# Performance work log

Hardware: AMD Instinct MI355X
Metric: run time of the kernel (lower is better)

The kernel has to match this reference:

```python
import jax, jax.numpy as jnp
import numpy as np
from jax import lax

N = 4096          # n_nodes
D_IN = 64         # node_attr_size
H = 64            # hidden_size
MAX_ITER = 10


def setup_inputs() -> dict:
    key = jax.random.key(0)
    ks = jax.random.split(key, 6)
    # Scale L and recurrent weights so the tanh fixed-point iteration is well-behaved
    X = jax.random.normal(ks[0], (N, D_IN), dtype=jnp.float32)
    L = jax.random.normal(ks[1], (N, N), dtype=jnp.float32) / jnp.sqrt(jnp.float32(N))
    W_ih0 = jax.random.normal(ks[2], (H, D_IN), dtype=jnp.float32) * 0.5
    W_hh0 = jax.random.normal(ks[3], (H, H), dtype=jnp.float32) * 0.5
    W_ih1 = jax.random.normal(ks[4], (H, H), dtype=jnp.float32) * 0.5
    W_hh1 = jax.random.normal(ks[5], (H, H), dtype=jnp.float32) * 0.5
    return {"X": X, "L": L, "W_ih0": W_ih0, "W_hh0": W_hh0,
            "W_ih1": W_ih1, "W_hh1": W_hh1}


def _gesn_layer(x, L, W_ih, W_hh):
    # wiu = linear(X, W_ih) computed once; then iterate
    # h <- tanh(wiu + L @ (h @ W_hh^T)) for max_iter steps (fixed-count
    # version of the torch convergence loop; see notes).
    wiu = x @ W_ih.T                                   # [N, H]
    h0 = jnp.zeros((x.shape[0], W_hh.shape[0]), x.dtype)

    def step(h, _):
        z = wiu + L @ (h @ W_hh.T)                     # [N, H]
        return jnp.tanh(z), None

    h, _ = lax.scan(step, h0, None, length=MAX_ITER)
    return h


def reference(X, L, W_ih0, W_hh0, W_ih1, W_hh1):
    h1 = _gesn_layer(X, L, W_ih0, W_hh0)               # layer 0: [N, H]
    h2 = _gesn_layer(h1, L, W_ih1, W_hh1)              # layer 1: [N, H]
    return jnp.concatenate([h1, h2], axis=-1)          # [N, 2H]
```

## Files before the change

### kernel.cpp

```cpp
#include <hip/hip_runtime.h>
#include <hip/hip_bf16.h>
#include <math.h>


#define NN 4096
#define HH 64

typedef float  f32x4  __attribute__((ext_vector_type(4)));
typedef short  bf16x8 __attribute__((ext_vector_type(8)));

static __device__ __forceinline__ unsigned short bf16_bits(__hip_bfloat16 b) {
    union { __hip_bfloat16 b; unsigned short u; } cv; cv.b = b; return cv.u;
}

__global__ __launch_bounds__(256) void convert_L(
    const float* __restrict__ L, short* __restrict__ Ahi, short* __restrict__ Alo)
{
    __shared__ float T[16 * 132];
    const int t  = threadIdx.x;
    const int rb = blockIdx.x >> 5;
    const int kg = blockIdx.x & 31;

    {
        const int row = t >> 4;
        const int c4  = (t & 15) * 4;
        const float* src = L + (size_t)(rb * 16 + row) * NN + kg * 128;
        float4 v0 = *reinterpret_cast<const float4*>(src + c4);
        float4 v1 = *reinterpret_cast<const float4*>(src + c4 + 64);
        *reinterpret_cast<float4*>(&T[row * 132 + c4])      = v0;
        *reinterpret_cast<float4*>(&T[row * 132 + c4 + 64]) = v1;
    }
    __syncthreads();

    const int kbl = t >> 6;
    const int l   = t & 63;
    const int r   = l & 15, g = l >> 4;
    short hi8[8], lo8[8];
#pragma unroll
    for (int j = 0; j < 8; ++j) {
        const float v = T[r * 132 + kbl * 32 + g * 8 + j];
        __hip_bfloat16 bh = __float2bfloat16(v);
        const float vh = __bfloat162float(bh);
        __hip_bfloat16 bl = __float2bfloat16(v - vh);
        hi8[j] = (short)bf16_bits(bh);
        lo8[j] = (short)bf16_bits(bl);
    }
    const size_t off = ((size_t)(rb * 128 + kg * 4 + kbl) * 64 + l) * 8;
    *reinterpret_cast<bf16x8*>(Ahi + off) = *reinterpret_cast<bf16x8*>(hi8);
    *reinterpret_cast<bf16x8*>(Alo + off) = *reinterpret_cast<bf16x8*>(lo8);
}

__global__ __launch_bounds__(512) void gesn_mm(
    const short* __restrict__ Ahi, const short* __restrict__ Alo,
    const short* __restrict__ Bhi, const short* __restrict__ Blo,
    float* __restrict__ Gp)
{
    __shared__ short Bh_lds[16 * 4 * 64 * 8];
    __shared__ short Bl_lds[16 * 4 * 64 * 8];

    const int t = threadIdx.x;
    const int w = t >> 6, l = t & 63;
    const int p = blockIdx.x >> 3;
    const int s = blockIdx.x & 7;
    const int rb = p * 8 + w;
    const int kb0 = s * 16;

    {
        const short* srcH = Bhi + (size_t)kb0 * 4 * 64 * 8;
        const short* srcL = Blo + (size_t)kb0 * 4 * 64 * 8;
#pragma unroll
        for (int q = 0; q < 8; ++q) {
            const int idx = (q * 512 + t) * 8;
            *reinterpret_cast<bf16x8*>(&Bh_lds[idx]) =
                *reinterpret_cast<const bf16x8*>(srcH + idx);
            *reinterpret_cast<bf16x8*>(&Bl_lds[idx]) =
                *reinterpret_cast<const bf16x8*>(srcL + idx);
        }
    }
    __syncthreads();

    const size_t abase = ((size_t)(rb * 128 + kb0) * 64 + l) * 8;
    bf16x8 aH[16], aL[16];
#pragma unroll
    for (int q = 0; q < 16; ++q) {
        aH[q] = *reinterpret_cast<const bf16x8*>(Ahi + abase + (size_t)q * 512);
        aL[q] = *reinterpret_cast<const bf16x8*>(Alo + abase + (size_t)q * 512);
    }

    f32x4 accP[4] = {};
    f32x4 accQ[4] = {};

#pragma unroll
    for (int kbl = 0; kbl < 16; ++kbl) {
        bf16x8 bH[4], bL[4];
#pragma unroll
        for (int cf = 0; cf < 4; ++cf) {
            const int idx = ((kbl * 4 + cf) * 64 + l) * 8;
            bH[cf] = *reinterpret_cast<const bf16x8*>(&Bh_lds[idx]);
            bL[cf] = *reinterpret_cast<const bf16x8*>(&Bl_lds[idx]);
        }
#pragma unroll
        for (int cf = 0; cf < 4; ++cf) {
            accP[cf] = __builtin_amdgcn_mfma_f32_16x16x32_bf16(
                aH[kbl], bH[cf], accP[cf], 0, 0, 0);
            accQ[cf] = __builtin_amdgcn_mfma_f32_16x16x32_bf16(
                aH[kbl], bL[cf], accQ[cf], 0, 0, 0);
            accQ[cf] = __builtin_amdgcn_mfma_f32_16x16x32_bf16(
                aL[kbl], bH[cf], accQ[cf], 0, 0, 0);
        }
    }

    float* g = Gp + (size_t)s * NN * HH;
    const int col0  = l & 15;
    const int rbase = (l >> 4) * 4;
#pragma unroll
    for (int cf = 0; cf < 4; ++cf)
#pragma unroll
        for (int r = 0; r < 4; ++r)
            g[(size_t)(rb * 16 + rbase + r) * HH + cf * 16 + col0]
                = accP[cf][r] + accQ[cf][r];
}

__global__ __launch_bounds__(256) void gesn_post(
    const float* __restrict__ Gsrc, int nsplit,
    const float* __restrict__ wiu_in, float* __restrict__ wiu_out,
    const float* __restrict__ W,
    float* __restrict__ hf32,
    short* __restrict__ Bhi, short* __restrict__ Blo,
    float* __restrict__ out2, int outc0)
{
    __shared__ float W_lds[64 * 65];
    __shared__ float G_lds[16 * 68];
    __shared__ unsigned short Hi_lds[16][66];
    __shared__ unsigned short Lo_lds[16][66];
    const int t = threadIdx.x;

    {
        const int j  = t >> 2;
        const int k0 = (t & 3) << 4;
#pragma unroll
        for (int q = 0; q < 16; ++q)
            W_lds[j * 65 + k0 + q] = W[j * 64 + k0 + q];
    }
    const int r0 = blockIdx.x * 16;

    {
        const int row = t >> 4;
        const int c4  = (t & 15) * 4;
        float4 sum;
        if (nsplit == 0) {
            sum = *reinterpret_cast<const float4*>(
                Gsrc + (size_t)(r0 + row) * HH + c4);
        } else {
            sum = make_float4(0.f, 0.f, 0.f, 0.f);
            for (int sidx = 0; sidx < nsplit; ++sidx) {
                const float4 v = *reinterpret_cast<const float4*>(
                    Gsrc + (size_t)sidx * NN * HH + (size_t)(r0 + row) * HH + c4);
                sum.x += v.x; sum.y += v.y; sum.z += v.z; sum.w += v.w;
            }
        }
        *reinterpret_cast<float4*>(&G_lds[row * 68 + c4]) = sum;
    }
    __syncthreads();

    const int j  = t & 63;
    const int ig = t >> 6;
#pragma unroll
    for (int rr = 0; rr < 4; ++rr) {
        const int i = ig * 4 + rr;
        float z = wiu_in ? wiu_in[(size_t)(r0 + i) * HH + j] : 0.f;
#pragma unroll
        for (int m = 0; m < 64; ++m)
            z = fmaf(G_lds[i * 68 + m], W_lds[j * 65 + m], z);
        if (wiu_out) wiu_out[(size_t)(r0 + i) * HH + j] = z;
        const float hv = tanhf(z);
        hf32[(size_t)(r0 + i) * HH + j] = hv;
        if (out2) out2[(size_t)(r0 + i) * 128 + outc0 + j] = hv;
        __hip_bfloat16 bh = __float2bfloat16(hv);
        const float vh = __bfloat162float(bh);
        __hip_bfloat16 bl = __float2bfloat16(hv - vh);
        Hi_lds[i][j] = bf16_bits(bh);
        Lo_lds[i][j] = bf16_bits(bl);
    }
    __syncthreads();

    if (t < 128) {
        const int j2     = t & 63;
        const int glocal = t >> 6;
        const int kb     = r0 >> 5;
        const int gg     = ((r0 & 31) >> 3) + glocal;
        const int cf     = j2 >> 4;
        const int lane   = gg * 16 + (j2 & 15);
        short hi8[8], lo8[8];
#pragma unroll
        for (int jj = 0; jj < 8; ++jj) {
            const int i = glocal * 8 + jj;
            hi8[jj] = (short)Hi_lds[i][j2];
            lo8[jj] = (short)Lo_lds[i][j2];
        }
        const size_t off = ((size_t)(kb * 4 + cf) * 64 + lane) * 8;
        *reinterpret_cast<bf16x8*>(Bhi + off) = *reinterpret_cast<bf16x8*>(hi8);
        *reinterpret_cast<bf16x8*>(Blo + off) = *reinterpret_cast<bf16x8*>(lo8);
    }
}

__global__ __launch_bounds__(256) void gesn_input_kernel(
    const float* __restrict__ x, const float* __restrict__ W,
    float* __restrict__ wiu, float* __restrict__ h)
{
    __shared__ float W_lds[64 * 65];
    __shared__ float x_lds[256];
    const int t = threadIdx.x;
    {
        const int j  = t >> 2;
        const int k0 = (t & 3) << 4;
#pragma unroll
        for (int q = 0; q < 16; ++q)
            W_lds[j * 65 + k0 + q] = W[j * 64 + k0 + q];
    }
    const int i0 = blockIdx.x * 4;
    x_lds[t] = x[i0 * 64 + t];
    __syncthreads();
    const int j = t & 63, i = t >> 6;
    float z = 0.f;
#pragma unroll
    for (int k = 0; k < 64; ++k)
        z = fmaf(x_lds[i * 64 + k], W_lds[j * 65 + k], z);
    const int gidx = (i0 + i) * 64 + j;
    wiu[gidx] = z;
    h[gidx]   = tanhf(z);
}

__global__ __launch_bounds__(256) void gesn_iter_kernel(
    const float* __restrict__ L, const float* __restrict__ h_in,
    const float* __restrict__ wiu, const float* __restrict__ W,
    float* __restrict__ h_out, float* __restrict__ out2, int out_col0)
{
    __shared__ float h_lds[64 * 64];
    __shared__ float L_lds[16 * 68];
    __shared__ float G_lds[16 * 68];
    __shared__ float W_lds[64 * 65];
    const int t = threadIdx.x;
    {
        const int j  = t >> 2;
        const int k0 = (t & 3) << 4;
#pragma unroll
        for (int q = 0; q < 16; ++q)
            W_lds[j * 65 + k0 + q] = W[j * 64 + k0 + q];
    }
    const int r0 = blockIdx.x * 16;
    const int p  = t >> 5;
    const int c0 = (t & 31) * 2;
    float acc00 = 0.f, acc01 = 0.f, acc10 = 0.f, acc11 = 0.f;
    const int lr = t >> 4;
    const int lc = (t & 15) * 4;
    for (int kb = 0; kb < 64; ++kb) {
        __syncthreads();
        const float4 lv = *reinterpret_cast<const float4*>(
            &L[(size_t)(r0 + lr) * 4096 + kb * 64 + lc]);
        *reinterpret_cast<float4*>(&L_lds[lr * 68 + lc]) = lv;
        const float4* hsrc = reinterpret_cast<const float4*>(h_in + kb * 4096);
        float4* hdst = reinterpret_cast<float4*>(h_lds);
#pragma unroll
        for (int q = 0; q < 4; ++q)
            hdst[t + 256 * q] = hsrc[t + 256 * q];
        __syncthreads();
#pragma unroll
        for (int kk = 0; kk < 64; ++kk) {
            const float  lv0 = L_lds[(2 * p) * 68 + kk];
            const float  lv1 = L_lds[(2 * p + 1) * 68 + kk];
            const float2 hv  = *reinterpret_cast<const float2*>(&h_lds[kk * 64 + c0]);
            acc00 = fmaf(lv0, hv.x, acc00);
            acc01 = fmaf(lv0, hv.y, acc01);
            acc10 = fmaf(lv1, hv.x, acc10);
            acc11 = fmaf(lv1, hv.y, acc11);
        }
    }
    G_lds[(2 * p) * 68 + c0]         = acc00;
    G_lds[(2 * p) * 68 + c0 + 1]     = acc01;
    G_lds[(2 * p + 1) * 68 + c0]     = acc10;
    G_lds[(2 * p + 1) * 68 + c0 + 1] = acc11;
    __syncthreads();
    const int j  = t & 63;
    const int iw = t >> 6;
#pragma unroll
    for (int rr = 0; rr < 4; ++rr) {
        const int i = iw * 4 + rr;
        float z = wiu[(size_t)(r0 + i) * 64 + j];
#pragma unroll
        for (int m = 0; m < 64; ++m)
            z = fmaf(G_lds[i * 68 + m], W_lds[j * 65 + m], z);
        const float hv = tanhf(z);
        h_out[(size_t)(r0 + i) * 64 + j] = hv;
        if (out2) out2[(size_t)(r0 + i) * 128 + out_col0 + j] = hv;
    }
}

extern "C" void kernel_launch(void* const* d_in, const int* in_sizes, int n_in,
                              void* d_out, int out_size, void* d_ws, size_t ws_size,
                              hipStream_t stream) {
    const float* X    = (const float*)d_in[0];
    const float* L    = (const float*)d_in[1];
    const float* Wih0 = (const float*)d_in[2];
    const float* Whh0 = (const float*)d_in[3];
    const float* Wih1 = (const float*)d_in[4];
    const float* Whh1 = (const float*)d_in[5];
    float* out = (float*)d_out;
    char* ws = (char*)d_ws;

    const size_t MB = 1024 * 1024;
    const size_t need = 76 * MB;

    if (ws_size >= need) {
        short* Ahi = (short*)(ws);
        short* Alo = (short*)(ws + 32 * MB);
        short* Bhi = (short*)(ws + 64 * MB);
        short* Blo = (short*)(ws + 64 * MB + 512 * 1024);
        float* wiu = (float*)(ws + 65 * MB);
        float* hA  = (float*)(ws + 66 * MB);
        float* hB  = (float*)(ws + 67 * MB);
        float* Gp  = (float*)(ws + 68 * MB);

        convert_L<<<8192, 256, 0, stream>>>(L, Ahi, Alo);

        for (int layer = 0; layer < 2; ++layer) {
            const float* x   = layer ? hA : X;
            const float* Wih = layer ? Wih1 : Wih0;
            const float* Whh = layer ? Whh1 : Whh0;
            float* hcur = layer ? hB : hA;

            gesn_post<<<256, 256, 0, stream>>>(x, 0, nullptr, wiu, Wih,
                                               hcur, Bhi, Blo, nullptr, 0);
            for (int it = 0; it < 9; ++it) {
                gesn_mm<<<256, 512, 0, stream>>>(Ahi, Alo, Bhi, Blo, Gp);
                float* o2 = (it == 8) ? out : nullptr;
                gesn_post<<<256, 256, 0, stream>>>(Gp, 8, wiu, nullptr, Whh,
                                                   hcur, Bhi, Blo, o2, layer * 64);
            }
        }
    } else {
        float* wiu = (float*)(ws);
        float* hA  = (float*)(ws + (1u << 20));
        float* hB  = (float*)(ws + (2u << 20));
        for (int layer = 0; layer < 2; ++layer) {
            const float* x   = layer ? hB : X;
            const float* Wih = layer ? Wih1 : Wih0;
            const float* Whh = layer ? Whh1 : Whh0;
            gesn_input_kernel<<<1024, 256, 0, stream>>>(x, Wih, wiu, hA);
            float* cur = hA;
            float* nxt = hB;
            for (int it = 0; it < 9; ++it) {
                float* o2 = (it == 8) ? out : nullptr;
                gesn_iter_kernel<<<256, 256, 0, stream>>>(L, cur, wiu, Whh, nxt,
                                                          o2, layer * 64);
                float* tmp = cur; cur = nxt; nxt = tmp;
            }
        }
    }
}
```

Baseline: 509.4 us.

## Fuse iteration loop into persistent kernel with grid barriers and register-resident L

Replaces the roughly 38 separate matmul and post-processing launches with one persistent 256-block kernel that steps through both layers and all iterations, separated by software grid barriers built on atomics. Each block loads its slice of the split-bf16 L once into registers and keeps it across all 18 matmul phases, so L is no longer re-read from memory every iteration. The post phase now runs with 512 threads, each handling 2 rows instead of 4. This relies on all 256 blocks being co-resident, since otherwise the spin barrier deadlocks. It also pays for barrier latency and holds large register and LDS allocations.

```diff
diff --git a/kernel.cpp b/kernel.cpp
--- a/kernel.cpp
+++ b/kernel.cpp
@@ -5,6 +5,8 @@
 
 #define NN 4096
 #define HH 64
+#define NBLK 256
+#define TPB 512
 
 typedef float  f32x4  __attribute__((ext_vector_type(4)));
 typedef short  bf16x8 __attribute__((ext_vector_type(8)));
@@ -50,101 +52,52 @@
     *reinterpret_cast<bf16x8*>(Alo + off) = *reinterpret_cast<bf16x8*>(lo8);
 }
 
-__global__ __launch_bounds__(512) void gesn_mm(
-    const short* __restrict__ Ahi, const short* __restrict__ Alo,
-    const short* __restrict__ Bhi, const short* __restrict__ Blo,
-    float* __restrict__ Gp)
-{
-    __shared__ short Bh_lds[16 * 4 * 64 * 8];
-    __shared__ short Bl_lds[16 * 4 * 64 * 8];
-
-    const int t = threadIdx.x;
-    const int w = t >> 6, l = t & 63;
-    const int p = blockIdx.x >> 3;
-    const int s = blockIdx.x & 7;
-    const int rb = p * 8 + w;
-    const int kb0 = s * 16;
-
-    {
-        const short* srcH = Bhi + (size_t)kb0 * 4 * 64 * 8;
-        const short* srcL = Blo + (size_t)kb0 * 4 * 64 * 8;
-#pragma unroll
-        for (int q = 0; q < 8; ++q) {
-            const int idx = (q * 512 + t) * 8;
-            *reinterpret_cast<bf16x8*>(&Bh_lds[idx]) =
-                *reinterpret_cast<const bf16x8*>(srcH + idx);
-            *reinterpret_cast<bf16x8*>(&Bl_lds[idx]) =
-                *reinterpret_cast<const bf16x8*>(srcL + idx);
-        }
-    }
-    __syncthreads();
-
-    const size_t abase = ((size_t)(rb * 128 + kb0) * 64 + l) * 8;
-    bf16x8 aH[16], aL[16];
-#pragma unroll
-    for (int q = 0; q < 16; ++q) {
-        aH[q] = *reinterpret_cast<const bf16x8*>(Ahi + abase + (size_t)q * 512);
-        aL[q] = *reinterpret_cast<const bf16x8*>(Alo + abase + (size_t)q * 512);
-    }
-
-    f32x4 accP[4] = {};
-    f32x4 accQ[4] = {};
-
-#pragma unroll
-    for (int kbl = 0; kbl < 16; ++kbl) {
-        bf16x8 bH[4], bL[4];
-#pragma unroll
-        for (int cf = 0; cf < 4; ++cf) {
-            const int idx = ((kbl * 4 + cf) * 64 + l) * 8;
-            bH[cf] = *reinterpret_cast<const bf16x8*>(&Bh_lds[idx]);
-            bL[cf] = *reinterpret_cast<const bf16x8*>(&Bl_lds[idx]);
-        }
-#pragma unroll
-        for (int cf = 0; cf < 4; ++cf) {
-            accP[cf] = __builtin_amdgcn_mfma_f32_16x16x32_bf16(
-                aH[kbl], bH[cf], accP[cf], 0, 0, 0);
-            accQ[cf] = __builtin_amdgcn_mfma_f32_16x16x32_bf16(
-                aH[kbl], bL[cf], accQ[cf], 0, 0, 0);
-            accQ[cf] = __builtin_amdgcn_mfma_f32_16x16x32_bf16(
-                aL[kbl], bH[cf], accQ[cf], 0, 0, 0);
-        }
-    }
-
-    float* g = Gp + (size_t)s * NN * HH;
-    const int col0  = l & 15;
-    const int rbase = (l >> 4) * 4;
-#pragma unroll
-    for (int cf = 0; cf < 4; ++cf)
-#pragma unroll
-        for (int r = 0; r < 4; ++r)
-            g[(size_t)(rb * 16 + rbase + r) * HH + cf * 16 + col0]
-                = accP[cf][r] + accQ[cf][r];
-}
-
-__global__ __launch_bounds__(256) void gesn_post(
+__device__ __forceinline__ void grid_barrier(unsigned* cnt, unsigned* gen, int nb)
+{
+    __syncthreads();
+    if (threadIdx.x == 0) {
+        __threadfence();
+        unsigned g = __hip_atomic_load(gen, __ATOMIC_RELAXED,
+                                       __HIP_MEMORY_SCOPE_AGENT);
+        unsigned old = __hip_atomic_fetch_add(cnt, 1u, __ATOMIC_ACQ_REL,
+                                              __HIP_MEMORY_SCOPE_AGENT);
+        if (old == (unsigned)(nb - 1)) {
+            __hip_atomic_store(cnt, 0u, __ATOMIC_RELAXED,
+                               __HIP_MEMORY_SCOPE_AGENT);
+            __hip_atomic_fetch_add(gen, 1u, __ATOMIC_RELEASE,
+                                   __HIP_MEMORY_SCOPE_AGENT);
+        } else {
+            while (__hip_atomic_load(gen, __ATOMIC_ACQUIRE,
+                                     __HIP_MEMORY_SCOPE_AGENT) == g) {
+                __builtin_amdgcn_s_sleep(2);
+            }
+        }
+        __threadfence();
+    }
+    __syncthreads();
+}
+
+__device__ __forceinline__ void post_phase(
     const float* __restrict__ Gsrc, int nsplit,
     const float* __restrict__ wiu_in, float* __restrict__ wiu_out,
-    const float* __restrict__ W,
-    float* __restrict__ hf32,
+    const float* __restrict__ W, float* __restrict__ hf32,
     short* __restrict__ Bhi, short* __restrict__ Blo,
-    float* __restrict__ out2, int outc0)
-{
-    __shared__ float W_lds[64 * 65];
-    __shared__ float G_lds[16 * 68];
-    __shared__ unsigned short Hi_lds[16][66];
-    __shared__ unsigned short Lo_lds[16][66];
+    float* __restrict__ out2, int outc0, int r0, char* smem)
+{
+    float* W_lds = (float*)smem;
+    float* G_lds = (float*)(smem + 16640);
+    unsigned short* Hi_lds = (unsigned short*)(smem + 16640 + 4352);
+    unsigned short* Lo_lds = (unsigned short*)(smem + 16640 + 4352 + 2112);
     const int t = threadIdx.x;
 
     {
-        const int j  = t >> 2;
-        const int k0 = (t & 3) << 4;
-#pragma unroll
-        for (int q = 0; q < 16; ++q)
+        const int j  = t >> 3;
+        const int k0 = (t & 7) * 8;
+#pragma unroll
+        for (int q = 0; q < 8; ++q)
             W_lds[j * 65 + k0 + q] = W[j * 64 + k0 + q];
     }
-    const int r0 = blockIdx.x * 16;
-
-    {
+    if (t < 256) {
         const int row = t >> 4;
         const int c4  = (t & 15) * 4;
         float4 sum;
@@ -166,8 +119,8 @@
     const int j  = t & 63;
     const int ig = t >> 6;
 #pragma unroll
-    for (int rr = 0; rr < 4; ++rr) {
-        const int i = ig * 4 + rr;
+    for (int rr = 0; rr < 2; ++rr) {
+        const int i = ig * 2 + rr;
         float z = wiu_in ? wiu_in[(size_t)(r0 + i) * HH + j] : 0.f;
 #pragma unroll
         for (int m = 0; m < 64; ++m)
@@ -179,8 +132,8 @@
         __hip_bfloat16 bh = __float2bfloat16(hv);
         const float vh = __bfloat162float(bh);
         __hip_bfloat16 bl = __float2bfloat16(hv - vh);
-        Hi_lds[i][j] = bf16_bits(bh);
-        Lo_lds[i][j] = bf16_bits(bl);
+        Hi_lds[i * 66 + j] = bf16_bits(bh);
+        Lo_lds[i * 66 + j] = bf16_bits(bl);
     }
     __syncthreads();
 
@@ -195,12 +148,107 @@
 #pragma unroll
         for (int jj = 0; jj < 8; ++jj) {
             const int i = glocal * 8 + jj;
-            hi8[jj] = (short)Hi_lds[i][j2];
-            lo8[jj] = (short)Lo_lds[i][j2];
+            hi8[jj] = (short)Hi_lds[i * 66 + j2];
+            lo8[jj] = (short)Lo_lds[i * 66 + j2];
         }
         const size_t off = ((size_t)(kb * 4 + cf) * 64 + lane) * 8;
         *reinterpret_cast<bf16x8*>(Bhi + off) = *reinterpret_cast<bf16x8*>(hi8);
         *reinterpret_cast<bf16x8*>(Blo + off) = *reinterpret_cast<bf16x8*>(lo8);
+    }
+}
+
+__global__ __launch_bounds__(TPB, 2) void gesn_persistent(
+    const short* __restrict__ Ahi, const short* __restrict__ Alo,
+    short* __restrict__ Bhi, short* __restrict__ Blo,
+    const float* __restrict__ X,
+    const float* __restrict__ Wih0, const float* __restrict__ Whh0,
+    const float* __restrict__ Wih1, const float* __restrict__ Whh1,
+    float* __restrict__ wiu, float* __restrict__ hA, float* __restrict__ hB,
+    float* __restrict__ Gp, float* __restrict__ out,
+    unsigned* bar_cnt, unsigned* bar_gen)
+{
+    __shared__ char smem[131072];
+    const int t = threadIdx.x;
+    const int b = blockIdx.x;
+    const int w = t >> 6, l = t & 63;
+    const int p = b >> 3, s = b & 7;
+    const int rb  = p * 8 + w;
+    const int kb0 = s * 16;
+    const int r0  = b * 16;
+
+    const size_t abase = ((size_t)(rb * 128 + kb0) * 64 + l) * 8;
+    bf16x8 aH[16], aL[16];
+#pragma unroll
+    for (int q = 0; q < 16; ++q) {
+        aH[q] = *reinterpret_cast<const bf16x8*>(Ahi + abase + (size_t)q * 512);
+        aL[q] = *reinterpret_cast<const bf16x8*>(Alo + abase + (size_t)q * 512);
+    }
+
+    for (int layer = 0; layer < 2; ++layer) {
+        const float* x   = layer ? hA : X;
+        const float* Wih = layer ? Wih1 : Wih0;
+        const float* Whh = layer ? Whh1 : Whh0;
+        float* hcur      = layer ? hB : hA;
+
+        post_phase(x, 0, nullptr, wiu, Wih, hcur, Bhi, Blo, nullptr, 0, r0, smem);
+        grid_barrier(bar_cnt, bar_gen, NBLK);
+
+        for (int it = 0; it < 9; ++it) {
+            short* Bh_lds = (short*)smem;
+            short* Bl_lds = (short*)(smem + 65536);
+            {
+                const short* srcH = Bhi + (size_t)kb0 * 4 * 64 * 8;
+                const short* srcL = Blo + (size_t)kb0 * 4 * 64 * 8;
+#pragma unroll
+                for (int q = 0; q < 8; ++q) {
+                    const int idx = (q * 512 + t) * 8;
+                    *reinterpret_cast<bf16x8*>(&Bh_lds[idx]) =
+                        *reinterpret_cast<const bf16x8*>(srcH + idx);
+                    *reinterpret_cast<bf16x8*>(&Bl_lds[idx]) =
+                        *reinterpret_cast<const bf16x8*>(srcL + idx);
+                }
+            }
+            __syncthreads();
+
+            f32x4 accP[4] = {};
+            f32x4 accQ[4] = {};
+#pragma unroll
+            for (int kbl = 0; kbl < 16; ++kbl) {
+                bf16x8 bH[4], bL[4];
+#pragma unroll
+                for (int cf = 0; cf < 4; ++cf) {
+                    const int idx = ((kbl * 4 + cf) * 64 + l) * 8;
+                    bH[cf] = *reinterpret_cast<const bf16x8*>(&Bh_lds[idx]);
+                    bL[cf] = *reinterpret_cast<const bf16x8*>(&Bl_lds[idx]);
+                }
+#pragma unroll
+                for (int cf = 0; cf < 4; ++cf) {
+                    accP[cf] = __builtin_amdgcn_mfma_f32_16x16x32_bf16(
+                        aH[kbl], bH[cf], accP[cf], 0, 0, 0);
+                    accQ[cf] = __builtin_amdgcn_mfma_f32_16x16x32_bf16(
+                        aH[kbl], bL[cf], accQ[cf], 0, 0, 0);
+                    accQ[cf] = __builtin_amdgcn_mfma_f32_16x16x32_bf16(
+                        aL[kbl], bH[cf], accQ[cf], 0, 0, 0);
+                }
+            }
+            {
+                float* g = Gp + (size_t)s * NN * HH;
+                const int col0  = l & 15;
+                const int rbase = (l >> 4) * 4;
+#pragma unroll
+                for (int cf = 0; cf < 4; ++cf)
+#pragma unroll
+                    for (int r = 0; r < 4; ++r)
+                        g[(size_t)(rb * 16 + rbase + r) * HH + cf * 16 + col0]
+                            = accP[cf][r] + accQ[cf][r];
+            }
+            grid_barrier(bar_cnt, bar_gen, NBLK);
+
+            float* o2 = (it == 8) ? out : nullptr;
+            post_phase(Gp, 8, wiu, nullptr, Whh, hcur, Bhi, Blo,
+                       o2, layer * 64, r0, smem);
+            grid_barrier(bar_cnt, bar_gen, NBLK);
+        }
     }
 }
 
@@ -309,7 +357,7 @@
     char* ws = (char*)d_ws;
 
     const size_t MB = 1024 * 1024;
-    const size_t need = 76 * MB;
+    const size_t need = 77 * MB;
 
     if (ws_size >= need) {
         short* Ahi = (short*)(ws);
@@ -320,24 +368,14 @@
         float* hA  = (float*)(ws + 66 * MB);
         float* hB  = (float*)(ws + 67 * MB);
         float* Gp  = (float*)(ws + 68 * MB);
-
+        unsigned char* bar = (unsigned char*)(ws + 76 * MB);
+
+        hipMemsetAsync(bar, 0, 1024, stream);
         convert_L<<<8192, 256, 0, stream>>>(L, Ahi, Alo);
-
-        for (int layer = 0; layer < 2; ++layer) {
-            const float* x   = layer ? hA : X;
-            const float* Wih = layer ? Wih1 : Wih0;
-            const float* Whh = layer ? Whh1 : Whh0;
-            float* hcur = layer ? hB : hA;
-
-            gesn_post<<<256, 256, 0, stream>>>(x, 0, nullptr, wiu, Wih,
-                                               hcur, Bhi, Blo, nullptr, 0);
-            for (int it = 0; it < 9; ++it) {
-                gesn_mm<<<256, 512, 0, stream>>>(Ahi, Alo, Bhi, Blo, Gp);
-                float* o2 = (it == 8) ? out : nullptr;
-                gesn_post<<<256, 256, 0, stream>>>(Gp, 8, wiu, nullptr, Whh,
-                                                   hcur, Bhi, Blo, o2, layer * 64);
-            }
-        }
+        gesn_persistent<<<NBLK, TPB, 0, stream>>>(
+            Ahi, Alo, Bhi, Blo, X, Wih0, Whh0, Wih1, Whh1,
+            wiu, hA, hB, Gp, out,
+            (unsigned*)bar, (unsigned*)(bar + 256));
     } else {
         float* wiu = (float*)(ws);
         float* hA  = (float*)(ws + (1u << 20));
```

After: 1.465 ms. 2.88x slower.

## Fuse split-K matmul and tanh update into one kernel per iteration

Applied to the files above, without the earlier changes.

Merges the split-K MFMA matmul and the post-processing kernel into one kernel per iteration. Each block owns 16 rows, its 8 waves split K, and partial sums are reduced in shared memory rather than through an 8-way global partial buffer. The packed bf16 h is double-buffered because other blocks still read the input h while this block writes its output. This removes a launch and the global round trip for partials, but each block now reads all of B straight from global/L2 with no LDS staging, and there are only 256 blocks.

```diff
diff --git a/kernel.cpp b/kernel.cpp
--- a/kernel.cpp
+++ b/kernel.cpp
@@ -50,137 +50,106 @@
     *reinterpret_cast<bf16x8*>(Alo + off) = *reinterpret_cast<bf16x8*>(lo8);
 }
 
-__global__ __launch_bounds__(512) void gesn_mm(
-    const short* __restrict__ Ahi, const short* __restrict__ Alo,
-    const short* __restrict__ Bhi, const short* __restrict__ Blo,
-    float* __restrict__ Gp)
-{
-    __shared__ short Bh_lds[16 * 4 * 64 * 8];
-    __shared__ short Bl_lds[16 * 4 * 64 * 8];
-
-    const int t = threadIdx.x;
-    const int w = t >> 6, l = t & 63;
-    const int p = blockIdx.x >> 3;
-    const int s = blockIdx.x & 7;
-    const int rb = p * 8 + w;
-    const int kb0 = s * 16;
-
-    {
-        const short* srcH = Bhi + (size_t)kb0 * 4 * 64 * 8;
-        const short* srcL = Blo + (size_t)kb0 * 4 * 64 * 8;
-#pragma unroll
-        for (int q = 0; q < 8; ++q) {
-            const int idx = (q * 512 + t) * 8;
-            *reinterpret_cast<bf16x8*>(&Bh_lds[idx]) =
-                *reinterpret_cast<const bf16x8*>(srcH + idx);
-            *reinterpret_cast<bf16x8*>(&Bl_lds[idx]) =
-                *reinterpret_cast<const bf16x8*>(srcL + idx);
-        }
-    }
-    __syncthreads();
-
-    const size_t abase = ((size_t)(rb * 128 + kb0) * 64 + l) * 8;
-    bf16x8 aH[16], aL[16];
-#pragma unroll
-    for (int q = 0; q < 16; ++q) {
-        aH[q] = *reinterpret_cast<const bf16x8*>(Ahi + abase + (size_t)q * 512);
-        aL[q] = *reinterpret_cast<const bf16x8*>(Alo + abase + (size_t)q * 512);
-    }
-
-    f32x4 accP[4] = {};
-    f32x4 accQ[4] = {};
-
-#pragma unroll
-    for (int kbl = 0; kbl < 16; ++kbl) {
-        bf16x8 bH[4], bL[4];
-#pragma unroll
-        for (int cf = 0; cf < 4; ++cf) {
-            const int idx = ((kbl * 4 + cf) * 64 + l) * 8;
-            bH[cf] = *reinterpret_cast<const bf16x8*>(&Bh_lds[idx]);
-            bL[cf] = *reinterpret_cast<const bf16x8*>(&Bl_lds[idx]);
-        }
-#pragma unroll
-        for (int cf = 0; cf < 4; ++cf) {
-            accP[cf] = __builtin_amdgcn_mfma_f32_16x16x32_bf16(
-                aH[kbl], bH[cf], accP[cf], 0, 0, 0);
-            accQ[cf] = __builtin_amdgcn_mfma_f32_16x16x32_bf16(
-                aH[kbl], bL[cf], accQ[cf], 0, 0, 0);
-            accQ[cf] = __builtin_amdgcn_mfma_f32_16x16x32_bf16(
-                aL[kbl], bH[cf], accQ[cf], 0, 0, 0);
-        }
-    }
-
-    float* g = Gp + (size_t)s * NN * HH;
-    const int col0  = l & 15;
-    const int rbase = (l >> 4) * 4;
-#pragma unroll
-    for (int cf = 0; cf < 4; ++cf)
-#pragma unroll
-        for (int r = 0; r < 4; ++r)
-            g[(size_t)(rb * 16 + rbase + r) * HH + cf * 16 + col0]
-                = accP[cf][r] + accQ[cf][r];
-}
-
-__global__ __launch_bounds__(256) void gesn_post(
-    const float* __restrict__ Gsrc, int nsplit,
-    const float* __restrict__ wiu_in, float* __restrict__ wiu_out,
-    const float* __restrict__ W,
+__global__ __launch_bounds__(512) void gesn_iter_fused(
+    const short* __restrict__ Ahi,  const short* __restrict__ Alo,
+    const short* __restrict__ BhiIn, const short* __restrict__ BloIn,
+    short* __restrict__ BhiOut, short* __restrict__ BloOut,
+    const float* __restrict__ wiu,  const float* __restrict__ W,
     float* __restrict__ hf32,
-    short* __restrict__ Bhi, short* __restrict__ Blo,
     float* __restrict__ out2, int outc0)
 {
     __shared__ float W_lds[64 * 65];
-    __shared__ float G_lds[16 * 68];
-    __shared__ unsigned short Hi_lds[16][66];
-    __shared__ unsigned short Lo_lds[16][66];
-    const int t = threadIdx.x;
-
-    {
-        const int j  = t >> 2;
-        const int k0 = (t & 3) << 4;
-#pragma unroll
-        for (int q = 0; q < 16; ++q)
+    __shared__ float Gpart[8][16 * 68];
+    __shared__ float Gred[16 * 68];
+    __shared__ unsigned short Hi_lds[16 * 66];
+    __shared__ unsigned short Lo_lds[16 * 66];
+
+    const int t  = threadIdx.x;
+    const int w  = t >> 6, l = t & 63;
+    const int b  = blockIdx.x;
+    const int rb = b;
+    const int r0 = b * 16;
+    const int kb0 = w * 16;
+
+    {
+        const int j  = t >> 3;
+        const int k0 = (t & 7) * 8;
+#pragma unroll
+        for (int q = 0; q < 8; ++q)
             W_lds[j * 65 + k0 + q] = W[j * 64 + k0 + q];
     }
-    const int r0 = blockIdx.x * 16;
-
-    {
-        const int row = t >> 4;
-        const int c4  = (t & 15) * 4;
-        float4 sum;
-        if (nsplit == 0) {
-            sum = *reinterpret_cast<const float4*>(
-                Gsrc + (size_t)(r0 + row) * HH + c4);
-        } else {
-            sum = make_float4(0.f, 0.f, 0.f, 0.f);
-            for (int sidx = 0; sidx < nsplit; ++sidx) {
-                const float4 v = *reinterpret_cast<const float4*>(
-                    Gsrc + (size_t)sidx * NN * HH + (size_t)(r0 + row) * HH + c4);
-                sum.x += v.x; sum.y += v.y; sum.z += v.z; sum.w += v.w;
-            }
-        }
-        *reinterpret_cast<float4*>(&G_lds[row * 68 + c4]) = sum;
+
+    const size_t abase = ((size_t)(rb * 128 + kb0) * 64 + l) * 8;
+    f32x4 accP[4] = {};
+    f32x4 accQ[4] = {};
+
+#pragma unroll
+    for (int kbl = 0; kbl < 16; ++kbl) {
+        const bf16x8 a_hi = *reinterpret_cast<const bf16x8*>(
+            Ahi + abase + (size_t)kbl * 512);
+        const bf16x8 a_lo = *reinterpret_cast<const bf16x8*>(
+            Alo + abase + (size_t)kbl * 512);
+        bf16x8 bH[4], bL[4];
+#pragma unroll
+        for (int cf = 0; cf < 4; ++cf) {
+            const size_t bo = ((size_t)((kb0 + kbl) * 4 + cf) * 64 + l) * 8;
+            bH[cf] = *reinterpret_cast<const bf16x8*>(BhiIn + bo);
+            bL[cf] = *reinterpret_cast<const bf16x8*>(BloIn + bo);
+        }
+#pragma unroll
+        for (int cf = 0; cf < 4; ++cf) {
+            accP[cf] = __builtin_amdgcn_mfma_f32_16x16x32_bf16(
+                a_hi, bH[cf], accP[cf], 0, 0, 0);
+            accQ[cf] = __builtin_amdgcn_mfma_f32_16x16x32_bf16(
+                a_hi, bL[cf], accQ[cf], 0, 0, 0);
+            accQ[cf] = __builtin_amdgcn_mfma_f32_16x16x32_bf16(
+                a_lo, bH[cf], accQ[cf], 0, 0, 0);
+        }
+    }
+
+    {
+        const int col0   = l & 15;
+        const int rbase4 = (l >> 4) * 4;
+#pragma unroll
+        for (int cf = 0; cf < 4; ++cf)
+#pragma unroll
+            for (int r = 0; r < 4; ++r)
+                Gpart[w][(rbase4 + r) * 68 + cf * 16 + col0]
+                    = accP[cf][r] + accQ[cf][r];
+    }
+    __syncthreads();
+
+    {
+        const int idx = t * 2;
+        const int i   = idx >> 6;
+        const int m   = idx & 63;
+        float2 sum = *reinterpret_cast<const float2*>(&Gpart[0][i * 68 + m]);
+#pragma unroll
+        for (int ww = 1; ww < 8; ++ww) {
+            const float2 v = *reinterpret_cast<const float2*>(&Gpart[ww][i * 68 + m]);
+            sum.x += v.x; sum.y += v.y;
+        }
+        *reinterpret_cast<float2*>(&Gred[i * 68 + m]) = sum;
     }
     __syncthreads();
 
     const int j  = t & 63;
     const int ig = t >> 6;
 #pragma unroll
-    for (int rr = 0; rr < 4; ++rr) {
-        const int i = ig * 4 + rr;
-        float z = wiu_in ? wiu_in[(size_t)(r0 + i) * HH + j] : 0.f;
+    for (int rr = 0; rr < 2; ++rr) {
+        const int i = ig * 2 + rr;
+        float z = wiu[(size_t)(r0 + i) * HH + j];
 #pragma unroll
         for (int m = 0; m < 64; ++m)
-            z = fmaf(G_lds[i * 68 + m], W_lds[j * 65 + m], z);
-        if (wiu_out) wiu_out[(size_t)(r0 + i) * HH + j] = z;
+            z = fmaf(Gred[i * 68 + m], W_lds[j * 65 + m], z);
         const float hv = tanhf(z);
         hf32[(size_t)(r0 + i) * HH + j] = hv;
         if (out2) out2[(size_t)(r0 + i) * 128 + outc0 + j] = hv;
         __hip_bfloat16 bh = __float2bfloat16(hv);
         const float vh = __bfloat162float(bh);
         __hip_bfloat16 bl = __float2bfloat16(hv - vh);
-        Hi_lds[i][j] = bf16_bits(bh);
-        Lo_lds[i][j] = bf16_bits(bl);
+        Hi_lds[i * 66 + j] = bf16_bits(bh);
+        Lo_lds[i * 66 + j] = bf16_bits(bl);
     }
     __syncthreads();
 
@@ -195,8 +164,76 @@
 #pragma unroll
         for (int jj = 0; jj < 8; ++jj) {
             const int i = glocal * 8 + jj;
-            hi8[jj] = (short)Hi_lds[i][j2];
-            lo8[jj] = (short)Lo_lds[i][j2];
+            hi8[jj] = (short)Hi_lds[i * 66 + j2];
+            lo8[jj] = (short)Lo_lds[i * 66 + j2];
+        }
+        const size_t off = ((size_t)(kb * 4 + cf) * 64 + lane) * 8;
+        *reinterpret_cast<bf16x8*>(BhiOut + off) = *reinterpret_cast<bf16x8*>(hi8);
+        *reinterpret_cast<bf16x8*>(BloOut + off) = *reinterpret_cast<bf16x8*>(lo8);
+    }
+}
+
+__global__ __launch_bounds__(256) void gesn_input_pack(
+    const float* __restrict__ x, float* __restrict__ wiu_out,
+    const float* __restrict__ W, float* __restrict__ hf32,
+    short* __restrict__ Bhi, short* __restrict__ Blo)
+{
+    __shared__ float W_lds[64 * 65];
+    __shared__ float G_lds[16 * 68];
+    __shared__ unsigned short Hi_lds[16 * 66];
+    __shared__ unsigned short Lo_lds[16 * 66];
+    const int t = threadIdx.x;
+
+    {
+        const int j  = t >> 2;
+        const int k0 = (t & 3) << 4;
+#pragma unroll
+        for (int q = 0; q < 16; ++q)
+            W_lds[j * 65 + k0 + q] = W[j * 64 + k0 + q];
+    }
+    const int r0 = blockIdx.x * 16;
+
+    {
+        const int row = t >> 4;
+        const int c4  = (t & 15) * 4;
+        *reinterpret_cast<float4*>(&G_lds[row * 68 + c4]) =
+            *reinterpret_cast<const float4*>(x + (size_t)(r0 + row) * HH + c4);
+    }
+    __syncthreads();
+
+    const int j  = t & 63;
+    const int ig = t >> 6;
+#pragma unroll
+    for (int rr = 0; rr < 4; ++rr) {
+        const int i = ig * 4 + rr;
+        float z = 0.f;
+#pragma unroll
+        for (int m = 0; m < 64; ++m)
+            z = fmaf(G_lds[i * 68 + m], W_lds[j * 65 + m], z);
+        wiu_out[(size_t)(r0 + i) * HH + j] = z;
+        const float hv = tanhf(z);
+        hf32[(size_t)(r0 + i) * HH + j] = hv;
+        __hip_bfloat16 bh = __float2bfloat16(hv);
+        const float vh = __bfloat162float(bh);
+        __hip_bfloat16 bl = __float2bfloat16(hv - vh);
+        Hi_lds[i * 66 + j] = bf16_bits(bh);
+        Lo_lds[i * 66 + j] = bf16_bits(bl);
+    }
+    __syncthreads();
+
+    if (t < 128) {
+        const int j2     = t & 63;
+        const int glocal = t >> 6;
+        const int kb     = r0 >> 5;
+        const int gg     = ((r0 & 31) >> 3) + glocal;
+        const int cf     = j2 >> 4;
+        const int lane   = gg * 16 + (j2 & 15);
+        short hi8[8], lo8[8];
+#pragma unroll
+        for (int jj = 0; jj < 8; ++jj) {
+            const int i = glocal * 8 + jj;
+            hi8[jj] = (short)Hi_lds[i * 66 + j2];
+            lo8[jj] = (short)Lo_lds[i * 66 + j2];
         }
         const size_t off = ((size_t)(kb * 4 + cf) * 64 + lane) * 8;
         *reinterpret_cast<bf16x8*>(Bhi + off) = *reinterpret_cast<bf16x8*>(hi8);
@@ -309,17 +346,18 @@
     char* ws = (char*)d_ws;
 
     const size_t MB = 1024 * 1024;
-    const size_t need = 76 * MB;
+    const size_t need = 72 * MB;
 
     if (ws_size >= need) {
-        short* Ahi = (short*)(ws);
-        short* Alo = (short*)(ws + 32 * MB);
-        short* Bhi = (short*)(ws + 64 * MB);
-        short* Blo = (short*)(ws + 64 * MB + 512 * 1024);
-        float* wiu = (float*)(ws + 65 * MB);
-        float* hA  = (float*)(ws + 66 * MB);
-        float* hB  = (float*)(ws + 67 * MB);
-        float* Gp  = (float*)(ws + 68 * MB);
+        short* Ahi  = (short*)(ws);
+        short* Alo  = (short*)(ws + 32 * MB);
+        short* BhiA = (short*)(ws + 64 * MB);
+        short* BloA = (short*)(ws + 64 * MB + 512 * 1024);
+        short* BhiB = (short*)(ws + 65 * MB);
+        short* BloB = (short*)(ws + 65 * MB + 512 * 1024);
+        float* wiu  = (float*)(ws + 66 * MB);
+        float* hA   = (float*)(ws + 67 * MB);
+        float* hB   = (float*)(ws + 68 * MB);
 
         convert_L<<<8192, 256, 0, stream>>>(L, Ahi, Alo);
 
@@ -327,15 +365,18 @@
             const float* x   = layer ? hA : X;
             const float* Wih = layer ? Wih1 : Wih0;
             const float* Whh = layer ? Whh1 : Whh0;
-            float* hcur = layer ? hB : hA;
-
-            gesn_post<<<256, 256, 0, stream>>>(x, 0, nullptr, wiu, Wih,
-                                               hcur, Bhi, Blo, nullptr, 0);
+            float* hcur      = layer ? hB : hA;
+
+            gesn_input_pack<<<256, 256, 0, stream>>>(x, wiu, Wih, hcur,
+                                                     BhiA, BloA);
+            short *bi_h = BhiA, *bi_l = BloA, *bo_h = BhiB, *bo_l = BloB;
             for (int it = 0; it < 9; ++it) {
-                gesn_mm<<<256, 512, 0, stream>>>(Ahi, Alo, Bhi, Blo, Gp);
                 float* o2 = (it == 8) ? out : nullptr;
-                gesn_post<<<256, 256, 0, stream>>>(Gp, 8, wiu, nullptr, Whh,
-                                                   hcur, Bhi, Blo, o2, layer * 64);
+                gesn_iter_fused<<<256, 512, 0, stream>>>(
+                    Ahi, Alo, bi_h, bi_l, bo_h, bo_l,
+                    wiu, Whh, hcur, o2, layer * 64);
+                short* th = bi_h; bi_h = bo_h; bo_h = th;
+                short* tl = bi_l; bi_l = bo_l; bo_l = tl;
             }
         }
     } else {
```

Result: slower. 561.4 us (+10.2%).
